# Kernel tuning notes

Hardware: AMD Instinct MI355X
Metric: run time of the kernel (lower is better)

The kernel has to match this reference:

```python
import jax, jax.numpy as jnp
import numpy as np

# Model hyperparameters (match init_kwargs)
N = 20000      # nodes
E = 320000     # edges (avg degree 16)
D = 128        # embed_dim
T = 8          # towers
F = D // T     # per-tower features = 16
L = 3          # num_layers
S = 4096       # number of subgraphs
INNER = (L + 1) * D  # concat of input + L layer outputs = 512
BN_EPS = 1e-5


def setup_inputs() -> dict:
    key = jax.random.key(0)
    ks = jax.random.split(key, 12)
    x = jax.random.normal(ks[0], (N, D), dtype=jnp.float32)
    edge_index = jax.random.randint(ks[1], (2, E), 0, N, dtype=jnp.int64)
    subgraph_indicator_index = jax.random.randint(ks[2], (N,), 0, S, dtype=jnp.int64)
    # Per-layer PNAConv params (stacked over L layers).
    # pre_nns: per tower Linear(2F -> F); post_nns: per tower Linear(2F -> F); lin: Linear(D -> D)
    pre_w = jax.random.normal(ks[3], (L, T, F, 2 * F), dtype=jnp.float32) / np.sqrt(2 * F)
    pre_b = jnp.zeros((L, T, F), dtype=jnp.float32)
    post_w = jax.random.normal(ks[4], (L, T, F, 2 * F), dtype=jnp.float32) / np.sqrt(2 * F)
    post_b = jnp.zeros((L, T, F), dtype=jnp.float32)
    lin_w = jax.random.normal(ks[5], (L, D, D), dtype=jnp.float32) / np.sqrt(D)
    lin_b = jnp.zeros((L, D), dtype=jnp.float32)
    # BatchNorm1d(INNER) in eval mode (running stats) + out_proj Linear(INNER -> D)
    bn_gamma = jnp.ones((INNER,), dtype=jnp.float32)
    bn_beta = jnp.zeros((INNER,), dtype=jnp.float32)
    bn_mean = jnp.zeros((INNER,), dtype=jnp.float32)
    bn_var = jnp.ones((INNER,), dtype=jnp.float32)
    op_w = jax.random.normal(ks[6], (D, INNER), dtype=jnp.float32) / np.sqrt(INNER)
    op_b = jnp.zeros((D,), dtype=jnp.float32)
    return {
        "x": x, "edge_index": edge_index,
        "subgraph_indicator_index": subgraph_indicator_index,
        "pre_w": pre_w, "pre_b": pre_b, "post_w": post_w, "post_b": post_b,
        "lin_w": lin_w, "lin_b": lin_b,
        "bn_gamma": bn_gamma, "bn_beta": bn_beta, "bn_mean": bn_mean, "bn_var": bn_var,
        "op_w": op_w, "op_b": op_b,
    }


def _pna_conv(h, src, dst, pre_w, pre_b, post_w, post_b, lin_w, lin_b):
    # PNAConv with aggregators=['sum'], scalers=['identity'], divide_input=True,
    # pre_layers=post_layers=1, no edge features.
    n = h.shape[0]
    xt = h.reshape(n, T, F)                                   # [N,T,F]
    # message: cat([x_i, x_j]) per edge, per-tower pre Linear
    msg_in = jnp.concatenate([xt[dst], xt[src]], axis=-1)     # [E,T,2F]
    m = jnp.einsum('etf,tgf->etg', msg_in, pre_w) + pre_b     # [E,T,F]
    # sum aggregation at target nodes
    agg = jax.ops.segment_sum(m, dst, num_segments=n)         # [N,T,F]
    # update: cat([x, agg]) -> per-tower post Linear -> flatten -> final Linear
    o = jnp.concatenate([xt, agg], axis=-1)                   # [N,T,2F]
    o = jnp.einsum('ntf,tgf->ntg', o, post_w) + post_b        # [N,T,F]
    return o.reshape(n, D) @ lin_w.T + lin_b                  # [N,D]


def reference(x, edge_index, subgraph_indicator_index,
              pre_w, pre_b, post_w, post_b, lin_w, lin_b,
              bn_gamma, bn_beta, bn_mean, bn_var, op_w, op_b):
    src = edge_index[0]  # x_j source
    dst = edge_index[1]  # x_i target / aggregation index
    x_cat = [x]
    h = x
    for l in range(L):
        h = jax.nn.relu(_pna_conv(h, src, dst, pre_w[l], pre_b[l],
                                  post_w[l], post_b[l], lin_w[l], lin_b[l]))
        x_cat.append(h)
    xc = jnp.concatenate(x_cat, axis=-1)                      # [N, (L+1)*D]
    pooled = jax.ops.segment_sum(xc, subgraph_indicator_index, num_segments=S)  # [S, INNER]
    xn = (pooled - bn_mean) * jax.lax.rsqrt(bn_var + BN_EPS) * bn_gamma + bn_beta
    return xn @ op_w.T + op_b                                  # [S, D]
```

## Files before the change

### kernel.cpp

```cpp
#include <hip/hip_runtime.h>
#include <cstdint>
#include <cstddef>

#define NN 20000
#define NE 320000
#define D  128
#define TW 8
#define FT 16
#define NL 3
#define NS 4096
#define INR 512

typedef unsigned short u16;
typedef __attribute__((ext_vector_type(8))) short short8;
typedef __attribute__((ext_vector_type(4))) float f32x4;

__device__ __forceinline__ float b2f(short s) {
    return __uint_as_float(((unsigned)(u16)s) << 16);
}
__device__ __forceinline__ u16 f2b(float f) {
    unsigned u = __float_as_uint(f);
    return (u16)((u + 0x7FFF + ((u >> 16) & 1)) >> 16);
}


__global__ void scan2_kernel(const int* __restrict__ cnt0, int* __restrict__ off0,
                             const int* __restrict__ cnt1, int* __restrict__ off1) {
    __shared__ int lds[1024];
    const int tid = threadIdx.x;
    const int* cnt = blockIdx.x ? cnt1 : cnt0;
    int*       off = blockIdx.x ? off1 : off0;
    const int n   = blockIdx.x ? NS : NN;
    const int per = (n + 1023) >> 10;
    const int s = tid * per;
    const int e = min(s + per, n);
    int sum = 0;
    for (int i = s; i < e; ++i) sum += cnt[i];
    lds[tid] = sum;
    __syncthreads();
    for (int o = 1; o < 1024; o <<= 1) {
        int v = (tid >= o) ? lds[tid - o] : 0;
        __syncthreads();
        if (tid >= o) lds[tid] += v;
        __syncthreads();
    }
    int base = (tid == 0) ? 0 : lds[tid - 1];
    for (int i = s; i < e; ++i) { off[i] = base; base += cnt[i]; }
    if (tid == 1023) off[n] = lds[1023];
}

__global__ void fill_kernel(const int* __restrict__ ei, const int* __restrict__ sub,
                            const int* __restrict__ eoff, int* __restrict__ ecur,
                            int* __restrict__ csr,
                            const int* __restrict__ soff, int* __restrict__ scur,
                            int* __restrict__ snodes) {
    int i = blockIdx.x * blockDim.x + threadIdx.x;
    if (i < NE) {
        int dd = ei[NE + i];
        int p = atomicAdd(&ecur[dd], 1);
        csr[eoff[dd] + p] = ei[i];
    }
    if (i < NN) {
        int g = sub[i];
        int p = atomicAdd(&scur[g], 1);
        snodes[soff[g] + p] = i;
    }
}

__global__ __launch_bounds__(256)
void prep_kernel(const float* __restrict__ pre_w, const float* __restrict__ pre_b,
                 const float* __restrict__ post_w,
                 float* __restrict__ cw, float* __restrict__ cv,
                 const float* __restrict__ op_w, const float* __restrict__ op_b,
                 const float* __restrict__ gma, const float* __restrict__ bta,
                 const float* __restrict__ mean, const float* __restrict__ var,
                 float* __restrict__ wefft, float* __restrict__ beff,
                 const float* __restrict__ lin_w, u16* __restrict__ packB,
                 const float* __restrict__ x, u16* __restrict__ xbf,
                 const int* __restrict__ ei, const int* __restrict__ sub,
                 int* __restrict__ deg, int* __restrict__ scnt) {
    const int b = blockIdx.x;
    const int tid = threadIdx.x;
    if (b < 24) {
        const int lt = b;
        const int dd = tid >> 4;
        const int ff = tid & 15;
        const float* PW = pre_w  + (size_t)lt * (FT * 2 * FT);
        const float* QW = post_w + (size_t)lt * (FT * 2 * FT);
        const float* PB = pre_b  + (size_t)lt * FT;
        float m1 = QW[dd * 32 + ff];
        float m2 = 0.f, m3 = 0.f, v = 0.f;
        for (int k = 0; k < FT; ++k) {
            float pb = QW[dd * 32 + 16 + k];
            m2 = fmaf(pb, PW[k * 32 + ff], m2);
            m3 = fmaf(pb, PW[k * 32 + 16 + ff], m3);
            if (ff == 0) v = fmaf(pb, PB[k], v);
        }
        float* o = cw + ((size_t)lt * 16 + dd) * 48;
        o[ff] = m1; o[16 + ff] = m2; o[32 + ff] = m3;
        if (ff == 0) cv[lt * 16 + dd] = v;
    } else if (b < 280) {
        int i = (b - 24) * 256 + tid;
        int j = i >> 7, d = i & (D - 1);
        float sc = gma[j] * rsqrtf(var[j] + 1e-5f);
        wefft[(size_t)j * D + d] = op_w[(size_t)d * INR + j] * sc;
    } else if (b < 312) {
        const int d = (b - 280) * 4 + (tid >> 6);
        const int lane = tid & 63;
        float acc = 0.f;
        for (int j = lane; j < INR; j += 64) {
            float sc = gma[j] * rsqrtf(var[j] + 1e-5f);
            float sh = bta[j] - mean[j] * sc;
            acc = fmaf(op_w[(size_t)d * INR + j], sh, acc);
        }
#pragma unroll
        for (int o = 32; o; o >>= 1) acc += __shfl_down(acc, o);
        if (lane == 0) beff[d] = acc + op_b[d];
    } else if (b < 336) {
        const int lt = b - 312;
        const int l  = lt >> 3, ct = lt & 7;
        const int ks = tid >> 6;
        const int lane = tid & 63;
        const int col = ct * 16 + (lane & 15);
        const int k0  = ks * 32 + ((lane >> 4) & 3) * 8;
        const float* lw = lin_w + (size_t)l * D * D + (size_t)col * D + k0;
        u16* o = packB + ((size_t)(lt * 4 + ks) * 64 + lane) * 8;
#pragma unroll
        for (int j = 0; j < 8; ++j) o[j] = f2b(lw[j]);
    } else if (b < 1586) {
        const size_t base = (size_t)(b - 336) * 2048 + (size_t)tid * 8;
        float4 a = *(const float4*)(x + base);
        float4 c = *(const float4*)(x + base + 4);
        u16 o[8] = { f2b(a.x), f2b(a.y), f2b(a.z), f2b(a.w),
                     f2b(c.x), f2b(c.y), f2b(c.z), f2b(c.w) };
        uint4 u;
        u.x = (unsigned)o[0] | ((unsigned)o[1] << 16);
        u.y = (unsigned)o[2] | ((unsigned)o[3] << 16);
        u.z = (unsigned)o[4] | ((unsigned)o[5] << 16);
        u.w = (unsigned)o[6] | ((unsigned)o[7] << 16);
        *(uint4*)(xbf + base) = u;
    } else {
        int i = (b - 1586) * 256 + tid;
        if (i < NE) atomicAdd(&deg[ei[NE + i]], 1);
        if (i < NN) atomicAdd(&scnt[sub[i]], 1);
    }
}

__global__ __launch_bounds__(512, 4)
void fgu_kernel(const u16* __restrict__ hin, const int* __restrict__ eoff,
                const int* __restrict__ csr, const int* __restrict__ deg,
                const float* __restrict__ cw, const float* __restrict__ cv,
                const float* __restrict__ post_b, const u16* __restrict__ packB,
                const float* __restrict__ lin_b, u16* __restrict__ hout, int l) {
    __shared__ float SG[16 * 128];
    __shared__ u16   XL[16 * 128];
    __shared__ u16   OBS[16 * 136];
    __shared__ float DG[16];

    const int tid  = threadIdx.x;
    const int lane = tid & 63;
    const int wv   = tid >> 6;
    const int n0   = blockIdx.x << 4;

    short8 BF[4];
    {
        const short8* pB = (const short8*)packB + (size_t)((l * 8 + wv) * 4) * 64 + lane;
#pragma unroll
        for (int ks = 0; ks < 4; ++ks) BF[ks] = pB[ks * 64];
    }
    const float bl = lin_b[l * D + wv * 16 + (lane & 15)];

    {
        const int half = lane >> 5;
        const int q    = lane & 31;
#pragma unroll
        for (int u = 0; u < 2; ++u) {
            const int ln = wv * 2 + u;
            const int node = n0 + ln;
            ((unsigned*)XL)[ln * 64 + lane] =
                ((const unsigned*)(hin + (size_t)node * D))[lane];
            if (lane == 0) DG[ln] = (float)deg[node];
            const int e0 = eoff[node], e1 = eoff[node + 1];
            const uint2* h2 = (const uint2*)hin;
            float ax = 0.f, ay = 0.f, az = 0.f, aw = 0.f;
            int e = e0;
            for (; e + 8 <= e1; e += 8) {
#pragma unroll
                for (int k = 0; k < 4; ++k) {
                    int s = csr[e + 2 * k + half];
                    uint2 v = h2[(size_t)s * 32 + q];
                    ax += __uint_as_float(v.x << 16);
                    ay += __uint_as_float(v.x & 0xFFFF0000u);
                    az += __uint_as_float(v.y << 16);
                    aw += __uint_as_float(v.y & 0xFFFF0000u);
                }
            }
            for (; e < e1; e += 2) {
                int idx = e + half;
                bool valid = idx < e1;
                int s = valid ? csr[idx] : 0;
                uint2 v = h2[(size_t)s * 32 + q];
                if (valid) {
                    ax += __uint_as_float(v.x << 16);
                    ay += __uint_as_float(v.x & 0xFFFF0000u);
                    az += __uint_as_float(v.y << 16);
                    aw += __uint_as_float(v.y & 0xFFFF0000u);
                }
            }
            ax += __shfl_xor(ax, 32);
            ay += __shfl_xor(ay, 32);
            az += __shfl_xor(az, 32);
            aw += __shfl_xor(aw, 32);
            if (half == 0) {
                float4 r; r.x = ax; r.y = ay; r.z = az; r.w = aw;
                ((float4*)SG)[ln * 32 + q] = r;
            }
        }
    }
    __syncthreads();

    {
        const int si  = tid >> 7;
        const int d   = tid & 127;
        const int t16 = d & ~15;
        const int dd  = d & 15;
        const float* wb = cw + ((size_t)(l * TW + (d >> 4)) * 16 + dd) * 48;
        const float4* wb4 = (const float4*)wb;
        float m1[16], m2[16], m3[16];
#pragma unroll
        for (int qq = 0; qq < 4; ++qq) {
            float4 t1 = wb4[qq], t2 = wb4[4 + qq], t3 = wb4[8 + qq];
            m1[qq*4+0]=t1.x; m1[qq*4+1]=t1.y; m1[qq*4+2]=t1.z; m1[qq*4+3]=t1.w;
            m2[qq*4+0]=t2.x; m2[qq*4+1]=t2.y; m2[qq*4+2]=t2.z; m2[qq*4+3]=t2.w;
            m3[qq*4+0]=t3.x; m3[qq*4+1]=t3.y; m3[qq*4+2]=t3.z; m3[qq*4+3]=t3.w;
        }
        const float vq = cv[(l * TW + (d >> 4)) * 16 + dd];
        const float cb = post_b[l * D + d];
#pragma unroll
        for (int u = 0; u < 4; ++u) {
            const int ln = si * 4 + u;
            const short8* hp = (const short8*)&XL[ln * 128 + t16];
            short8 hx0 = hp[0], hx1 = hp[1];
            const float4* sp = (const float4*)&SG[ln * 128 + t16];
            float4 sv0 = sp[0], sv1 = sp[1], sv2 = sp[2], sv3 = sp[3];
            float ax = 0.f, am = 0.f, as2 = 0.f;
#pragma unroll
            for (int j = 0; j < 8; ++j) {
                float xf = b2f(hx0[j]);
                ax = fmaf(m1[j], xf, ax);
                am = fmaf(m2[j], xf, am);
            }
#pragma unroll
            for (int j = 0; j < 8; ++j) {
                float xf = b2f(hx1[j]);
                ax = fmaf(m1[8 + j], xf, ax);
                am = fmaf(m2[8 + j], xf, am);
            }
            as2 = fmaf(m3[0], sv0.x, as2); as2 = fmaf(m3[1], sv0.y, as2);
            as2 = fmaf(m3[2], sv0.z, as2); as2 = fmaf(m3[3], sv0.w, as2);
            as2 = fmaf(m3[4], sv1.x, as2); as2 = fmaf(m3[5], sv1.y, as2);
            as2 = fmaf(m3[6], sv1.z, as2); as2 = fmaf(m3[7], sv1.w, as2);
            as2 = fmaf(m3[8], sv2.x, as2); as2 = fmaf(m3[9], sv2.y, as2);
            as2 = fmaf(m3[10], sv2.z, as2); as2 = fmaf(m3[11], sv2.w, as2);
            as2 = fmaf(m3[12], sv3.x, as2); as2 = fmaf(m3[13], sv3.y, as2);
            as2 = fmaf(m3[14], sv3.z, as2); as2 = fmaf(m3[15], sv3.w, as2);
            OBS[ln * 136 + d] = f2b(cb + ax + as2 + DG[ln] * (am + vq));
        }
    }
    __syncthreads();

    f32x4 c = {0.f, 0.f, 0.f, 0.f};
#pragma unroll
    for (int ks = 0; ks < 4; ++ks) {
        const short8 a = *(const short8*)((const char*)OBS +
                            (lane & 15) * 272 + (ks * 4 + (lane >> 4)) * 16);
        c = __builtin_amdgcn_mfma_f32_16x16x32_bf16(a, BF[ks], c, 0, 0, 0);
    }
    const int d_epi = wv * 16 + (lane & 15);
#pragma unroll
    for (int r = 0; r < 4; ++r) {
        const int node = n0 + (lane >> 4) * 4 + r;
        float v = fmaxf(c[r] + bl, 0.f);
        hout[(size_t)node * D + d_epi] = f2b(v);
    }
}

__global__ __launch_bounds__(512)
void pool_out_kernel(const u16* __restrict__ h0, const u16* __restrict__ h1,
                     const u16* __restrict__ h2, const u16* __restrict__ h3,
                     const int* __restrict__ soff, const int* __restrict__ snodes,
                     const float* __restrict__ wefft, const float* __restrict__ beff,
                     float* __restrict__ out) {
    __shared__ float sm[16 * INR];
    const int tid = threadIdx.x;
    const int q = tid >> 7;
    const int d = tid & 127;
    const int s0 = blockIdx.x * 16;
    const u16* hq = (q == 0) ? h0 : (q == 1) ? h1 : (q == 2) ? h2 : h3;
    for (int i = 0; i < 16; ++i) {
        const int a0 = soff[s0 + i], a1 = soff[s0 + i + 1];
        float acc = 0.f;
        for (int a = a0; a < a1; ++a) {
            int n = snodes[a];
            acc += b2f(hq[(size_t)n * D + d]);
        }
        sm[i * INR + q * 128 + d] = acc;
    }
    __syncthreads();
    float acc[16];
#pragma unroll
    for (int i = 0; i < 16; ++i) acc[i] = 0.f;
    for (int jj4 = 0; jj4 < 32; ++jj4) {
        const int j0 = q * 128 + jj4 * 4;
        float wv0 = wefft[(size_t)(j0 + 0) * D + d];
        float wv1 = wefft[(size_t)(j0 + 1) * D + d];
        float wv2 = wefft[(size_t)(j0 + 2) * D + d];
        float wv3 = wefft[(size_t)(j0 + 3) * D + d];
#pragma unroll
        for (int i = 0; i < 16; ++i) {
            float4 pv = *(const float4*)&sm[i * INR + j0];
            acc[i] = fmaf(pv.x, wv0, acc[i]);
            acc[i] = fmaf(pv.y, wv1, acc[i]);
            acc[i] = fmaf(pv.z, wv2, acc[i]);
            acc[i] = fmaf(pv.w, wv3, acc[i]);
        }
    }
    __syncthreads();
#pragma unroll
    for (int i = 0; i < 16; ++i) sm[(q * 16 + i) * 128 + d] = acc[i];
    __syncthreads();
    const float bb = beff[d];
#pragma unroll
    for (int ii = 0; ii < 4; ++ii) {
        int i = q * 4 + ii;
        float v = sm[i * 128 + d] + sm[(16 + i) * 128 + d]
                + sm[(32 + i) * 128 + d] + sm[(48 + i) * 128 + d];
        out[(size_t)(s0 + i) * D + d] = v + bb;
    }
}


extern "C" void kernel_launch(void* const* d_in, const int* in_sizes, int n_in,
                              void* d_out, int out_size, void* d_ws, size_t ws_size,
                              hipStream_t stream) {
    const float* x      = (const float*)d_in[0];
    const int*   ei     = (const int*)d_in[1];
    const int*   sub    = (const int*)d_in[2];
    const float* pre_w  = (const float*)d_in[3];
    const float* pre_b  = (const float*)d_in[4];
    const float* post_w = (const float*)d_in[5];
    const float* post_b = (const float*)d_in[6];
    const float* lin_w  = (const float*)d_in[7];
    const float* lin_b  = (const float*)d_in[8];
    const float* bn_g   = (const float*)d_in[9];
    const float* bn_b   = (const float*)d_in[10];
    const float* bn_m   = (const float*)d_in[11];
    const float* bn_v   = (const float*)d_in[12];
    const float* op_w   = (const float*)d_in[13];
    const float* op_b   = (const float*)d_in[14];
    float* out = (float*)d_out;

    char* p = (char*)d_ws;
    auto alloc = [&](size_t bytes) -> char* {
        char* q = p;
        p += (bytes + 255) & ~(size_t)255;
        return q;
    };

    char* zero_start = p;
    int* deg  = (int*)alloc(sizeof(int) * NN);
    int* ecur = (int*)alloc(sizeof(int) * NN);
    int* scnt = (int*)alloc(sizeof(int) * NS);
    int* scur = (int*)alloc(sizeof(int) * NS);
    size_t zero_span = (size_t)(p - zero_start);

    int* eoff   = (int*)alloc(sizeof(int) * (NN + 1));
    int* soff   = (int*)alloc(sizeof(int) * (NS + 1));
    int* csr    = (int*)alloc(sizeof(int) * NE);
    int* snodes = (int*)alloc(sizeof(int) * NN);
    u16* xbf    = (u16*)alloc(sizeof(u16) * (size_t)NN * D);
    u16* h1     = (u16*)alloc(sizeof(u16) * (size_t)NN * D);
    u16* h2     = (u16*)alloc(sizeof(u16) * (size_t)NN * D);
    u16* h3     = (u16*)alloc(sizeof(u16) * (size_t)NN * D);
    float* wefft  = (float*)alloc(sizeof(float) * (size_t)INR * D);
    float* beff   = (float*)alloc(sizeof(float) * D);
    float* cw     = (float*)alloc(sizeof(float) * NL * TW * 16 * 48);
    float* cv     = (float*)alloc(sizeof(float) * NL * TW * 16);
    u16* packB    = (u16*)alloc(sizeof(u16) * NL * 8 * 4 * 64 * 8);

    hipMemsetAsync(zero_start, 0, zero_span, stream);

    prep_kernel<<<2836, 256, 0, stream>>>(pre_w, pre_b, post_w, cw, cv,
                                          op_w, op_b, bn_g, bn_b, bn_m, bn_v,
                                          wefft, beff, lin_w, packB, x, xbf,
                                          ei, sub, deg, scnt);
    scan2_kernel<<<2, 1024, 0, stream>>>(deg, eoff, scnt, soff);
    fill_kernel<<<(NE + 255) / 256, 256, 0, stream>>>(ei, sub, eoff, ecur, csr,
                                                      soff, scur, snodes);

    const u16* hs[4] = { xbf, h1, h2, h3 };
    for (int l = 0; l < NL; ++l) {
        fgu_kernel<<<NN / 16, 512, 0, stream>>>(hs[l], eoff, csr, deg, cw, cv,
                                                post_b, packB, lin_b,
                                                (u16*)hs[l + 1], l);
    }

    pool_out_kernel<<<NS / 16, 512, 0, stream>>>(xbf, h1, h2, h3, soff, snodes,
                                                 wefft, beff, out);
}
```

Baseline: 299.2 us.

## Fuse subgraph pooling into layer kernels via float atomics

Subgraph sum-pooling moves out of the final kernel. Each node's features are now atomically added into an fp32 pooled buffer: the x→bf16 conversion pass does this for the input features, and each layer kernel's epilogue does it for that layer's output. The final kernel only loads the pooled rows and applies the folded BN and out_proj weights, and the last layer no longer writes h3. This removes the gather-based pooling pass and one hidden-state write, but adds about 10M fp32 atomics spread over a 2M-entry buffer. It also pools in fp32 instead of the bf16-rounded hidden states, and it zeroes a larger workspace span with the memset.

Result: slower. 351.6 us (+17.5%).

```diff
diff --git a/kernel.cpp b/kernel.cpp
--- a/kernel.cpp
+++ b/kernel.cpp
@@ -78,7 +78,8 @@
                  const float* __restrict__ lin_w, u16* __restrict__ packB,
                  const float* __restrict__ x, u16* __restrict__ xbf,
                  const int* __restrict__ ei, const int* __restrict__ sub,
-                 int* __restrict__ deg, int* __restrict__ scnt) {
+                 int* __restrict__ deg, int* __restrict__ scnt,
+                 float* __restrict__ pooled) {
     const int b = blockIdx.x;
     const int tid = threadIdx.x;
     if (b < 24) {
@@ -129,6 +130,8 @@
         for (int j = 0; j < 8; ++j) o[j] = f2b(lw[j]);
     } else if (b < 1586) {
         const size_t base = (size_t)(b - 336) * 2048 + (size_t)tid * 8;
+        const int node = (int)(base >> 7);
+        const int d0   = (int)(base & 127);
         float4 a = *(const float4*)(x + base);
         float4 c = *(const float4*)(x + base + 4);
         u16 o[8] = { f2b(a.x), f2b(a.y), f2b(a.z), f2b(a.w),
@@ -139,6 +142,11 @@
         u.z = (unsigned)o[4] | ((unsigned)o[5] << 16);
         u.w = (unsigned)o[6] | ((unsigned)o[7] << 16);
         *(uint4*)(xbf + base) = u;
+        float* pb = pooled + (size_t)sub[node] * INR + d0;
+        atomicAdd(pb + 0, a.x); atomicAdd(pb + 1, a.y);
+        atomicAdd(pb + 2, a.z); atomicAdd(pb + 3, a.w);
+        atomicAdd(pb + 4, c.x); atomicAdd(pb + 5, c.y);
+        atomicAdd(pb + 6, c.z); atomicAdd(pb + 7, c.w);
     } else {
         int i = (b - 1586) * 256 + tid;
         if (i < NE) atomicAdd(&deg[ei[NE + i]], 1);
@@ -149,13 +157,16 @@
 __global__ __launch_bounds__(512, 4)
 void fgu_kernel(const u16* __restrict__ hin, const int* __restrict__ eoff,
                 const int* __restrict__ csr, const int* __restrict__ deg,
+                const int* __restrict__ sub,
                 const float* __restrict__ cw, const float* __restrict__ cv,
                 const float* __restrict__ post_b, const u16* __restrict__ packB,
-                const float* __restrict__ lin_b, u16* __restrict__ hout, int l) {
+                const float* __restrict__ lin_b, u16* __restrict__ hout,
+                float* __restrict__ pooled, int l) {
     __shared__ float SG[16 * 128];
     __shared__ u16   XL[16 * 128];
     __shared__ u16   OBS[16 * 136];
     __shared__ float DG[16];
+    __shared__ int   SUBL[16];
 
     const int tid  = threadIdx.x;
     const int lane = tid & 63;
@@ -169,6 +180,7 @@
         for (int ks = 0; ks < 4; ++ks) BF[ks] = pB[ks * 64];
     }
     const float bl = lin_b[l * D + wv * 16 + (lane & 15)];
+    if (tid < 16) SUBL[tid] = sub[n0 + tid];
 
     {
         const int half = lane >> 5;
@@ -277,34 +289,30 @@
         c = __builtin_amdgcn_mfma_f32_16x16x32_bf16(a, BF[ks], c, 0, 0, 0);
     }
     const int d_epi = wv * 16 + (lane & 15);
+    const bool write_h = (l < NL - 1);
+    float* pcol = pooled + (size_t)(l + 1) * 128 + d_epi;
 #pragma unroll
     for (int r = 0; r < 4; ++r) {
-        const int node = n0 + (lane >> 4) * 4 + r;
+        const int ln = (lane >> 4) * 4 + r;
+        const int node = n0 + ln;
         float v = fmaxf(c[r] + bl, 0.f);
-        hout[(size_t)node * D + d_epi] = f2b(v);
+        if (write_h) hout[(size_t)node * D + d_epi] = f2b(v);
+        atomicAdd(pcol + (size_t)SUBL[ln] * INR, v);
     }
 }
 
 __global__ __launch_bounds__(512)
-void pool_out_kernel(const u16* __restrict__ h0, const u16* __restrict__ h1,
-                     const u16* __restrict__ h2, const u16* __restrict__ h3,
-                     const int* __restrict__ soff, const int* __restrict__ snodes,
-                     const float* __restrict__ wefft, const float* __restrict__ beff,
-                     float* __restrict__ out) {
+void out_kernel(const float* __restrict__ pooled, const float* __restrict__ wefft,
+                const float* __restrict__ beff, float* __restrict__ out) {
     __shared__ float sm[16 * INR];
     const int tid = threadIdx.x;
     const int q = tid >> 7;
     const int d = tid & 127;
     const int s0 = blockIdx.x * 16;
-    const u16* hq = (q == 0) ? h0 : (q == 1) ? h1 : (q == 2) ? h2 : h3;
-    for (int i = 0; i < 16; ++i) {
-        const int a0 = soff[s0 + i], a1 = soff[s0 + i + 1];
-        float acc = 0.f;
-        for (int a = a0; a < a1; ++a) {
-            int n = snodes[a];
-            acc += b2f(hq[(size_t)n * D + d]);
-        }
-        sm[i * INR + q * 128 + d] = acc;
+    {
+        const float4* src = (const float4*)(pooled + (size_t)s0 * INR);
+        float4* dst = (float4*)sm;
+        for (int i = tid; i < 16 * INR / 4; i += 512) dst[i] = src[i];
     }
     __syncthreads();
     float acc[16];
@@ -372,6 +380,7 @@
     int* ecur = (int*)alloc(sizeof(int) * NN);
     int* scnt = (int*)alloc(sizeof(int) * NS);
     int* scur = (int*)alloc(sizeof(int) * NS);
+    float* pooled = (float*)alloc(sizeof(float) * (size_t)NS * INR);
     size_t zero_span = (size_t)(p - zero_start);
 
     int* eoff   = (int*)alloc(sizeof(int) * (NN + 1));
@@ -381,7 +390,6 @@
     u16* xbf    = (u16*)alloc(sizeof(u16) * (size_t)NN * D);
     u16* h1     = (u16*)alloc(sizeof(u16) * (size_t)NN * D);
     u16* h2     = (u16*)alloc(sizeof(u16) * (size_t)NN * D);
-    u16* h3     = (u16*)alloc(sizeof(u16) * (size_t)NN * D);
     float* wefft  = (float*)alloc(sizeof(float) * (size_t)INR * D);
     float* beff   = (float*)alloc(sizeof(float) * D);
     float* cw     = (float*)alloc(sizeof(float) * NL * TW * 16 * 48);
@@ -393,18 +401,17 @@
     prep_kernel<<<2836, 256, 0, stream>>>(pre_w, pre_b, post_w, cw, cv,
                                           op_w, op_b, bn_g, bn_b, bn_m, bn_v,
                                           wefft, beff, lin_w, packB, x, xbf,
-                                          ei, sub, deg, scnt);
+                                          ei, sub, deg, scnt, pooled);
     scan2_kernel<<<2, 1024, 0, stream>>>(deg, eoff, scnt, soff);
     fill_kernel<<<(NE + 255) / 256, 256, 0, stream>>>(ei, sub, eoff, ecur, csr,
                                                       soff, scur, snodes);
 
-    const u16* hs[4] = { xbf, h1, h2, h3 };
+    const u16* hs[4] = { xbf, h1, h2, h1  };
     for (int l = 0; l < NL; ++l) {
-        fgu_kernel<<<NN / 16, 512, 0, stream>>>(hs[l], eoff, csr, deg, cw, cv,
-                                                post_b, packB, lin_b,
-                                                (u16*)hs[l + 1], l);
-    }
-
-    pool_out_kernel<<<NS / 16, 512, 0, stream>>>(xbf, h1, h2, h3, soff, snodes,
-                                                 wefft, beff, out);
-}
+        fgu_kernel<<<NN / 16, 512, 0, stream>>>(hs[l], eoff, csr, deg, sub,
+                                                cw, cv, post_b, packB, lin_b,
+                                                (u16*)hs[l + 1], pooled, l);
+    }
+
+    out_kernel<<<NS / 16, 512, 0, stream>>>(pooled, wefft, beff, out);
+}
```

## Split pooling into wide-parallel kernel and unroll neighbor gather to 16 edges

Applied to the files above, without the earlier changes.

The fused pool+projection kernel is split in two. A new pool kernel runs one block per subgraph and reads 4 bf16 values per lane, replacing the old 256-block kernel that walked 16 subgraphs serially with scalar loads. The projection kernel now reads the pooled fp32 buffer from global memory. Separately, the edge-gather loop in the layer kernel is unrolled to 16 edges with all loads issued before the adds, to expose more memory-level parallelism. The cost is an extra 8 MB pooled buffer round trip, one more launch, and higher register pressure in the gather.

Measured after the change: 273.7 us. 8.5% less time.

```diff
diff --git a/kernel.cpp b/kernel.cpp
--- a/kernel.cpp
+++ b/kernel.cpp
@@ -173,6 +173,7 @@
     {
         const int half = lane >> 5;
         const int q    = lane & 31;
+        const uint2* h2 = (const uint2*)hin;
 #pragma unroll
         for (int u = 0; u < 2; ++u) {
             const int ln = wv * 2 + u;
@@ -181,19 +182,54 @@
                 ((const unsigned*)(hin + (size_t)node * D))[lane];
             if (lane == 0) DG[ln] = (float)deg[node];
             const int e0 = eoff[node], e1 = eoff[node + 1];
-            const uint2* h2 = (const uint2*)hin;
             float ax = 0.f, ay = 0.f, az = 0.f, aw = 0.f;
             int e = e0;
-            for (; e + 8 <= e1; e += 8) {
-#pragma unroll
-                for (int k = 0; k < 4; ++k) {
-                    int s = csr[e + 2 * k + half];
-                    uint2 v = h2[(size_t)s * 32 + q];
-                    ax += __uint_as_float(v.x << 16);
-                    ay += __uint_as_float(v.x & 0xFFFF0000u);
-                    az += __uint_as_float(v.y << 16);
-                    aw += __uint_as_float(v.y & 0xFFFF0000u);
-                }
+            for (; e + 16 <= e1; e += 16) {
+                int s0 = csr[e +  0 + half], s1 = csr[e +  2 + half];
+                int s2 = csr[e +  4 + half], s3 = csr[e +  6 + half];
+                int s4 = csr[e +  8 + half], s5 = csr[e + 10 + half];
+                int s6 = csr[e + 12 + half], s7 = csr[e + 14 + half];
+                uint2 v0 = h2[(size_t)s0 * 32 + q];
+                uint2 v1 = h2[(size_t)s1 * 32 + q];
+                uint2 v2 = h2[(size_t)s2 * 32 + q];
+                uint2 v3 = h2[(size_t)s3 * 32 + q];
+                uint2 v4 = h2[(size_t)s4 * 32 + q];
+                uint2 v5 = h2[(size_t)s5 * 32 + q];
+                uint2 v6 = h2[(size_t)s6 * 32 + q];
+                uint2 v7 = h2[(size_t)s7 * 32 + q];
+                ax += __uint_as_float(v0.x << 16) + __uint_as_float(v1.x << 16)
+                    + __uint_as_float(v2.x << 16) + __uint_as_float(v3.x << 16)
+                    + __uint_as_float(v4.x << 16) + __uint_as_float(v5.x << 16)
+                    + __uint_as_float(v6.x << 16) + __uint_as_float(v7.x << 16);
+                ay += __uint_as_float(v0.x & 0xFFFF0000u) + __uint_as_float(v1.x & 0xFFFF0000u)
+                    + __uint_as_float(v2.x & 0xFFFF0000u) + __uint_as_float(v3.x & 0xFFFF0000u)
+                    + __uint_as_float(v4.x & 0xFFFF0000u) + __uint_as_float(v5.x & 0xFFFF0000u)
+                    + __uint_as_float(v6.x & 0xFFFF0000u) + __uint_as_float(v7.x & 0xFFFF0000u);
+                az += __uint_as_float(v0.y << 16) + __uint_as_float(v1.y << 16)
+                    + __uint_as_float(v2.y << 16) + __uint_as_float(v3.y << 16)
+                    + __uint_as_float(v4.y << 16) + __uint_as_float(v5.y << 16)
+                    + __uint_as_float(v6.y << 16) + __uint_as_float(v7.y << 16);
+                aw += __uint_as_float(v0.y & 0xFFFF0000u) + __uint_as_float(v1.y & 0xFFFF0000u)
+                    + __uint_as_float(v2.y & 0xFFFF0000u) + __uint_as_float(v3.y & 0xFFFF0000u)
+                    + __uint_as_float(v4.y & 0xFFFF0000u) + __uint_as_float(v5.y & 0xFFFF0000u)
+                    + __uint_as_float(v6.y & 0xFFFF0000u) + __uint_as_float(v7.y & 0xFFFF0000u);
+            }
+            if (e + 8 <= e1) {
+                int s0 = csr[e + 0 + half], s1 = csr[e + 2 + half];
+                int s2 = csr[e + 4 + half], s3 = csr[e + 6 + half];
+                uint2 v0 = h2[(size_t)s0 * 32 + q];
+                uint2 v1 = h2[(size_t)s1 * 32 + q];
+                uint2 v2 = h2[(size_t)s2 * 32 + q];
+                uint2 v3 = h2[(size_t)s3 * 32 + q];
+                ax += __uint_as_float(v0.x << 16) + __uint_as_float(v1.x << 16)
+                    + __uint_as_float(v2.x << 16) + __uint_as_float(v3.x << 16);
+                ay += __uint_as_float(v0.x & 0xFFFF0000u) + __uint_as_float(v1.x & 0xFFFF0000u)
+                    + __uint_as_float(v2.x & 0xFFFF0000u) + __uint_as_float(v3.x & 0xFFFF0000u);
+                az += __uint_as_float(v0.y << 16) + __uint_as_float(v1.y << 16)
+                    + __uint_as_float(v2.y << 16) + __uint_as_float(v3.y << 16);
+                aw += __uint_as_float(v0.y & 0xFFFF0000u) + __uint_as_float(v1.y & 0xFFFF0000u)
+                    + __uint_as_float(v2.y & 0xFFFF0000u) + __uint_as_float(v3.y & 0xFFFF0000u);
+                e += 8;
             }
             for (; e < e1; e += 2) {
                 int idx = e + half;
@@ -285,26 +321,54 @@
     }
 }
 
+
+__global__ __launch_bounds__(128)
+void pool_kernel(const u16* __restrict__ h0, const u16* __restrict__ h1,
+                 const u16* __restrict__ h2, const u16* __restrict__ h3,
+                 const int* __restrict__ soff, const int* __restrict__ snodes,
+                 float* __restrict__ pooled) {
+    const int s = blockIdx.x;
+    const int t = threadIdx.x;
+    const int seg = t >> 5, q = t & 31;
+    const u16* hs = (seg == 0) ? h0 : (seg == 1) ? h1 : (seg == 2) ? h2 : h3;
+    const uint2* hv = (const uint2*)hs;
+    const int a0 = soff[s], a1 = soff[s + 1];
+    float ax = 0.f, ay = 0.f, az = 0.f, aw = 0.f;
+    int a = a0;
+    for (; a + 2 <= a1; a += 2) {
+        int na = snodes[a], nb = snodes[a + 1];
+        uint2 va = hv[(size_t)na * 32 + q];
+        uint2 vb = hv[(size_t)nb * 32 + q];
+        ax += __uint_as_float(va.x << 16) + __uint_as_float(vb.x << 16);
+        ay += __uint_as_float(va.x & 0xFFFF0000u) + __uint_as_float(vb.x & 0xFFFF0000u);
+        az += __uint_as_float(va.y << 16) + __uint_as_float(vb.y << 16);
+        aw += __uint_as_float(va.y & 0xFFFF0000u) + __uint_as_float(vb.y & 0xFFFF0000u);
+    }
+    if (a < a1) {
+        int n = snodes[a];
+        uint2 v = hv[(size_t)n * 32 + q];
+        ax += __uint_as_float(v.x << 16);
+        ay += __uint_as_float(v.x & 0xFFFF0000u);
+        az += __uint_as_float(v.y << 16);
+        aw += __uint_as_float(v.y & 0xFFFF0000u);
+    }
+    float4 r; r.x = ax; r.y = ay; r.z = az; r.w = aw;
+    ((float4*)pooled)[(size_t)s * 128 + seg * 32 + q] = r;
+}
+
+
 __global__ __launch_bounds__(512)
-void pool_out_kernel(const u16* __restrict__ h0, const u16* __restrict__ h1,
-                     const u16* __restrict__ h2, const u16* __restrict__ h3,
-                     const int* __restrict__ soff, const int* __restrict__ snodes,
-                     const float* __restrict__ wefft, const float* __restrict__ beff,
-                     float* __restrict__ out) {
+void out_kernel(const float* __restrict__ pooled, const float* __restrict__ wefft,
+                const float* __restrict__ beff, float* __restrict__ out) {
     __shared__ float sm[16 * INR];
     const int tid = threadIdx.x;
     const int q = tid >> 7;
     const int d = tid & 127;
     const int s0 = blockIdx.x * 16;
-    const u16* hq = (q == 0) ? h0 : (q == 1) ? h1 : (q == 2) ? h2 : h3;
-    for (int i = 0; i < 16; ++i) {
-        const int a0 = soff[s0 + i], a1 = soff[s0 + i + 1];
-        float acc = 0.f;
-        for (int a = a0; a < a1; ++a) {
-            int n = snodes[a];
-            acc += b2f(hq[(size_t)n * D + d]);
-        }
-        sm[i * INR + q * 128 + d] = acc;
+    {
+        const float4* src = (const float4*)(pooled + (size_t)s0 * INR);
+        float4* dst = (float4*)sm;
+        for (int i = tid; i < 16 * INR / 4; i += 512) dst[i] = src[i];
     }
     __syncthreads();
     float acc[16];
@@ -382,6 +446,7 @@
     u16* h1     = (u16*)alloc(sizeof(u16) * (size_t)NN * D);
     u16* h2     = (u16*)alloc(sizeof(u16) * (size_t)NN * D);
     u16* h3     = (u16*)alloc(sizeof(u16) * (size_t)NN * D);
+    float* pooled = (float*)alloc(sizeof(float) * (size_t)NS * INR);
     float* wefft  = (float*)alloc(sizeof(float) * (size_t)INR * D);
     float* beff   = (float*)alloc(sizeof(float) * D);
     float* cw     = (float*)alloc(sizeof(float) * NL * TW * 16 * 48);
@@ -405,6 +470,6 @@
                                                 (u16*)hs[l + 1], l);
     }
 
-    pool_out_kernel<<<NS / 16, 512, 0, stream>>>(xbf, h1, h2, h3, soff, snodes,
-                                                 wefft, beff, out);
-}
+    pool_kernel<<<NS, 128, 0, stream>>>(xbf, h1, h2, h3, soff, snodes, pooled);
+    out_kernel<<<NS / 16, 512, 0, stream>>>(pooled, wefft, beff, out);
+}
```
